# Performance work log

Measured on AMD Instinct MI355X. Metric: run time of the kernel, lower is better.

Reference implementation:

```python
import jax, jax.numpy as jnp
import numpy as np

NUM_EMBED = 1024
NUM_HEADS = 16
NUM_LAYER = 8
BLOCK_SIZE = 1024
VOCAB = 32000
B, T = 4, 1024
HEAD_SIZE = NUM_EMBED // NUM_HEADS


def _ln(x, g, b, eps=1e-5):
    mu = jnp.mean(x, axis=-1, keepdims=True)
    var = jnp.var(x, axis=-1, keepdims=True)
    return (x - mu) * jax.lax.rsqrt(var + eps) * g + b


def setup_inputs() -> dict:
    key = jax.random.key(0)
    ks = jax.random.split(key, 16)
    C, L, V = NUM_EMBED, NUM_LAYER, VOCAB
    std = 0.02
    n = lambda k, shp: jax.random.normal(k, shp, jnp.float32) * std
    return {
        "x": jax.random.randint(ks[0], (B, T), 0, V),
        "tok_emb": n(ks[1], (V, C)),
        "pos_emb": n(ks[2], (BLOCK_SIZE, C)),
        "Wq": n(ks[3], (L, C, C)),
        "Wk": n(ks[4], (L, C, C)),
        "Wv": n(ks[5], (L, C, C)),
        "Wproj": n(ks[6], (L, C, C)),
        "bproj": jnp.zeros((L, C), jnp.float32),
        "ln1_g": jnp.ones((L, C), jnp.float32),
        "ln1_b": jnp.zeros((L, C), jnp.float32),
        "ln2_g": jnp.ones((L, C), jnp.float32),
        "ln2_b": jnp.zeros((L, C), jnp.float32),
        "W1": n(ks[7], (L, C, 4 * C)),
        "b1": jnp.zeros((L, 4 * C), jnp.float32),
        "W2": n(ks[8], (L, 4 * C, C)),
        "b2": jnp.zeros((L, C), jnp.float32),
        "lnf_g": jnp.ones((C,), jnp.float32),
        "lnf_b": jnp.zeros((C,), jnp.float32),
        "Whead": n(ks[9], (C, V)),
    }


def _forward(x, tok_emb, pos_emb, Wq, Wk, Wv, Wproj, bproj,
             ln1_g, ln1_b, ln2_g, ln2_b, W1, b1, W2, b2,
             lnf_g, lnf_b, Whead):
    Bc, Tc = x.shape
    H, hs = NUM_HEADS, HEAD_SIZE
    h = tok_emb[x] + pos_emb[:Tc]  # [B,T,C]
    causal = jnp.tril(jnp.ones((Tc, Tc), bool))
    neg_inf = jnp.finfo(h.dtype).min
    for l in range(NUM_LAYER):
        xn = _ln(h, ln1_g[l], ln1_b[l])
        q = (xn @ Wq[l]).reshape(Bc, Tc, H, hs)
        k = (xn @ Wk[l]).reshape(Bc, Tc, H, hs)
        v = (xn @ Wv[l]).reshape(Bc, Tc, H, hs)
        att = jnp.einsum('bqhd,bkhd->bhqk', q, k) * (hs ** -0.5)
        att = jnp.where(causal, att, neg_inf)
        att = jax.nn.softmax(att, axis=-1)  # dropout p=0 in eval
        o = jnp.einsum('bhqk,bkhd->bqhd', att, v).reshape(Bc, Tc, H * hs)
        h = h + o @ Wproj[l] + bproj[l]
        xn = _ln(h, ln2_g[l], ln2_b[l])
        h = h + jax.nn.relu(xn @ W1[l] + b1[l]) @ W2[l] + b2[l]
    h = _ln(h, lnf_g, lnf_b)
    return h @ Whead  # logits [B,T,V]


def reference(x, tok_emb, pos_emb, Wq, Wk, Wv, Wproj, bproj,
              ln1_g, ln1_b, ln2_g, ln2_b, W1, b1, W2, b2,
              lnf_g, lnf_b, Whead):
    return _forward(x, tok_emb, pos_emb, Wq, Wk, Wv, Wproj, bproj,
                    ln1_g, ln1_b, ln2_g, ln2_b, W1, b1, W2, b2,
                    lnf_g, lnf_b, Whead)
```

## Files before the change

kernel.cpp:

```cpp
#include <hip/hip_runtime.h>
#include <stdint.h>
#include <stddef.h>

#define C_DIM 1024
#define T_DIM 1024
#define B_DIM 4
#define L_DIM 8
#define V_DIM 32000
#define HS 64
#define NHEAD 16
#define NROWS (B_DIM * T_DIM)
#define LDQ   3072

typedef __bf16 bf16_t;
typedef __attribute__((ext_vector_type(8))) __bf16 bf16x8;
typedef __attribute__((ext_vector_type(4))) __bf16 bf16x4;
typedef __attribute__((ext_vector_type(4))) float f32x4;
typedef unsigned int u32;
typedef unsigned short u16;

static __device__ __forceinline__ f32x4 mfma16(bf16x8 a, bf16x8 b, f32x4 c) {
    return __builtin_amdgcn_mfma_f32_16x16x32_bf16(a, b, c, 0, 0, 0);
}

static __device__ __forceinline__ void gl_lds16(const bf16_t* g, bf16_t* l) {
    __builtin_amdgcn_global_load_lds(
        (const __attribute__((address_space(1))) u32*)(const void*)g,
        (__attribute__((address_space(3))) u32*)(void*)l, 16, 0, 0);
}

__global__ __launch_bounds__(256) void embed_kernel(
    const int* __restrict__ x, const float* __restrict__ tok,
    const float* __restrict__ pos, float* __restrict__ h) {
    int idx = blockIdx.x * 256 + threadIdx.x;
    int row = idx >> 8;
    int c4  = (idx & 255) * 4;
    int t   = row & (T_DIM - 1);
    int tk  = x[row];
    float4 a = *(const float4*)(tok + (size_t)tk * C_DIM + c4);
    float4 p = *(const float4*)(pos + (size_t)t * C_DIM + c4);
    float4 r;
    r.x = a.x + p.x; r.y = a.y + p.y; r.z = a.z + p.z; r.w = a.w + p.w;
    *(float4*)(h + (size_t)row * C_DIM + c4) = r;
}

static __device__ __forceinline__ void wtr_tile(
    const float* __restrict__ in, bf16_t* __restrict__ out,
    int K, int N, int n0, int k0, int tid) {
    __shared__ float t[64][65];
    int tx = tid & 63, tw = tid >> 6;
#pragma unroll 4
    for (int i = 0; i < 16; ++i) {
        int k = tw * 16 + i;
        t[k][tx] = in[(size_t)(k0 + k) * N + n0 + tx];
    }
    __syncthreads();
#pragma unroll 4
    for (int i = 0; i < 16; ++i) {
        int n = tw * 16 + i;
        out[(size_t)(n0 + n) * K + k0 + tx] = (bf16_t)t[tx][n];
    }
}

__global__ __launch_bounds__(256) void wtr_kernel(
    const float* __restrict__ in, bf16_t* __restrict__ out, int K, int N) {
    wtr_tile(in, out, K, N, blockIdx.x * 64, blockIdx.y * 64, threadIdx.x);
}

__global__ __launch_bounds__(256) void wtr_layer_kernel(
    const float* __restrict__ Wq, const float* __restrict__ Wk,
    const float* __restrict__ Wv, const float* __restrict__ Wp,
    const float* __restrict__ W1, const float* __restrict__ W2,
    bf16_t* __restrict__ qkvT, bf16_t* __restrict__ projT,
    bf16_t* __restrict__ w1T, bf16_t* __restrict__ w2T) {
    int b = blockIdx.x;
    const float* in; bf16_t* out; int K, N, tn, tk;
    if (b < 1024) {
        int which = b >> 8, t = b & 255;
        in  = which == 0 ? Wq : which == 1 ? Wk : which == 2 ? Wv : Wp;
        out = which < 3 ? qkvT + (size_t)which * C_DIM * C_DIM : projT;
        K = C_DIM; N = C_DIM; tn = t & 15; tk = t >> 4;
    } else if (b < 2048) {
        int t = b - 1024; in = W1; out = w1T;
        K = C_DIM; N = 4 * C_DIM; tn = t & 63; tk = t >> 6;
    } else {
        int t = b - 2048; in = W2; out = w2T;
        K = 4 * C_DIM; N = C_DIM; tn = t & 15; tk = t >> 4;
    }
    wtr_tile(in, out, K, N, tn * 64, tk * 64, threadIdx.x);
}

__global__ __launch_bounds__(256) void ln_kernel(
    const float* __restrict__ x, const float* __restrict__ gam,
    const float* __restrict__ bet, bf16_t* __restrict__ out) {
    int wave = threadIdx.x >> 6, lane = threadIdx.x & 63;
    int row  = blockIdx.x * 4 + wave;
    const float* xr = x + (size_t)row * C_DIM;
    float4 v[4];
    float s = 0.f, sq = 0.f;
#pragma unroll
    for (int i = 0; i < 4; ++i) {
        v[i] = *(const float4*)(xr + i * 256 + lane * 4);
        s  += v[i].x + v[i].y + v[i].z + v[i].w;
        sq += v[i].x * v[i].x + v[i].y * v[i].y + v[i].z * v[i].z + v[i].w * v[i].w;
    }
#pragma unroll
    for (int m = 1; m < 64; m <<= 1) {
        s  += __shfl_xor(s, m);
        sq += __shfl_xor(sq, m);
    }
    float mu  = s * (1.f / 1024.f);
    float var = sq * (1.f / 1024.f) - mu * mu;
    float rs  = rsqrtf(var + 1e-5f);
    bf16_t* orow = out + (size_t)row * C_DIM;
#pragma unroll
    for (int i = 0; i < 4; ++i) {
        int c = i * 256 + lane * 4;
        float4 g4 = *(const float4*)(gam + c);
        float4 b4 = *(const float4*)(bet + c);
        bf16x4 o;
        o[0] = (bf16_t)((v[i].x - mu) * rs * g4.x + b4.x);
        o[1] = (bf16_t)((v[i].y - mu) * rs * g4.y + b4.y);
        o[2] = (bf16_t)((v[i].z - mu) * rs * g4.z + b4.z);
        o[3] = (bf16_t)((v[i].w - mu) * rs * g4.w + b4.w);
        *(bf16x4*)(orow + c) = o;
    }
}

template <int MODE>
__global__ __launch_bounds__(256) void gemm_kernel(
    const bf16_t* __restrict__ A, const bf16_t* __restrict__ Bt,
    const float* __restrict__ bias, void* __restrict__ Cout,
    int M, int N, int K) {
    __shared__ bf16_t Asm[2][128 * 32];
    __shared__ bf16_t Bsm[2][128 * 32];

    const int tid  = threadIdx.x;
    const int nwg  = gridDim.x;
    int bid = blockIdx.x;
    if ((nwg & 7) == 0) {
        int cpx = nwg >> 3;
        bid = (bid & 7) * cpx + (bid >> 3);
    }
    const int MT = M >> 7;
    const int mt = bid % MT, nt = bid / MT;
    const int mbase = mt << 7, nbase = nt << 7;
    const int wave = tid >> 6, lane = tid & 63;
    const int lr = lane & 15, lg = lane >> 4;
    const int wm = wave >> 1, wn = wave & 1;
    const int NK = K >> 5;

    const int srow = lane >> 2;
    const int ssw  = (((lane & 3) ^ ((lane >> 3) & 3)) << 3);
    const bf16_t* aRow = A  + (size_t)(mbase + wave * 32 + srow) * K + ssw;
    const bf16_t* bRow = Bt + (size_t)(nbase + wave * 32 + srow) * K + ssw;
    const int ldsW = wave * 1024;

#define STAGE(buf, kt)                                                        \
    do {                                                                      \
        const bf16_t* ag = aRow + (size_t)(kt) * 32;                          \
        const bf16_t* bg = bRow + (size_t)(kt) * 32;                          \
        gl_lds16(ag,            &Asm[buf][ldsW]);                             \
        gl_lds16(ag + 16 * K,   &Asm[buf][ldsW + 512]);                       \
        gl_lds16(bg,            &Bsm[buf][ldsW]);                             \
        gl_lds16(bg + 16 * K,   &Bsm[buf][ldsW + 512]);                       \
    } while (0)

    STAGE(0, 0);
    __syncthreads();

    f32x4 acc[4][4] = {};
    const int rsw = ((lg ^ ((lr >> 1) & 3)) << 3);
    int buf = 0;
    for (int kt = 0; kt < NK; ++kt) {
        if (kt + 1 < NK) STAGE(buf ^ 1, kt + 1);
        bf16x8 af[4], bfr[4];
#pragma unroll
        for (int i = 0; i < 4; ++i)
            af[i] = *(const bf16x8*)&Asm[buf][(wm * 64 + i * 16 + lr) * 32 + rsw];
#pragma unroll
        for (int j = 0; j < 4; ++j)
            bfr[j] = *(const bf16x8*)&Bsm[buf][(wn * 64 + j * 16 + lr) * 32 + rsw];
#pragma unroll
        for (int i = 0; i < 4; ++i)
#pragma unroll
            for (int j = 0; j < 4; ++j)
                acc[i][j] = mfma16(af[i], bfr[j], acc[i][j]);
        __syncthreads();
        buf ^= 1;
    }
#undef STAGE

    float bj[4];
#pragma unroll
    for (int j = 0; j < 4; ++j)
        bj[j] = bias ? bias[nbase + wn * 64 + j * 16 + lr] : 0.0f;
#pragma unroll
    for (int i = 0; i < 4; ++i) {
#pragma unroll
        for (int j = 0; j < 4; ++j) {
            int col = nbase + wn * 64 + j * 16 + lr;
#pragma unroll
            for (int e = 0; e < 4; ++e) {
                int row = mbase + wm * 64 + i * 16 + lg * 4 + e;
                float val = acc[i][j][e] + bj[j];
                size_t off = (size_t)row * N + col;
                if (MODE == 0) {
                    ((bf16_t*)Cout)[off] = (bf16_t)val;
                } else if (MODE == 1) {
                    ((bf16_t*)Cout)[off] = (bf16_t)fmaxf(val, 0.0f);
                } else if (MODE == 2) {
                    ((float*)Cout)[off] += val;
                } else {
                    __builtin_nontemporal_store(val, &((float*)Cout)[off]);
                }
            }
        }
    }
}

template <int MODE>
__global__ __launch_bounds__(512, 2) void gemm256_kernel(
    const bf16_t* __restrict__ A, const bf16_t* __restrict__ Bt,
    const float* __restrict__ bias, void* __restrict__ Cout,
    int M, int N, int K) {
    __shared__ bf16_t As[2][256 * 64];
    __shared__ bf16_t Bs[2][256 * 64];

    const int tid  = threadIdx.x;
    const int nwg  = gridDim.x;
    int bid = blockIdx.x;
    if ((nwg & 7) == 0) {
        int cpx = nwg >> 3;
        bid = (bid & 7) * cpx + (bid >> 3);
    }
    const int MT = M >> 8;
    const int mt = bid % MT, nt = bid / MT;
    const int mbase = mt << 8, nbase = nt << 8;
    const int wave = tid >> 6, lane = tid & 63;
    const int lr = lane & 15, lg = lane >> 4;
    const int wm128 = (wave >> 2) * 128;
    const int wn64  = (wave & 3) * 64;
    const int NT = K >> 6;

    const int ssw = (((tid & 7) ^ ((tid >> 3) & 7)) << 3);
    const bf16_t* aRow = A  + (size_t)(mbase + (tid >> 3)) * K + ssw;
    const bf16_t* bRow = Bt + (size_t)(nbase + (tid >> 3)) * K + ssw;
    const int ldsW = wave * 8 * 64;

#pragma unroll
    for (int i = 0; i < 4; ++i) {
        gl_lds16(aRow + (size_t)i * 64 * K, &As[0][i * 64 * 64 + ldsW]);
        gl_lds16(bRow + (size_t)i * 64 * K, &Bs[0][i * 64 * 64 + ldsW]);
    }
    asm volatile("s_waitcnt vmcnt(0)" ::: "memory");
    __builtin_amdgcn_s_barrier();
    asm volatile("" ::: "memory");

    f32x4 acc[8][4] = {};

    for (int t = 0; t < NT; ++t) {
        const int cur = t & 1, nxt = cur ^ 1;
        const bool pf = (t + 1 < NT);
#pragma unroll
        for (int q = 0; q < 4; ++q) {
            bf16x8 af[2][2], bfr[2][4];
#pragma unroll
            for (int h = 0; h < 2; ++h) {
                const int c = h * 4 + lg;
#pragma unroll
                for (int dm = 0; dm < 2; ++dm) {
                    int row = wm128 + (2 * q + dm) * 16 + lr;
                    af[h][dm] = *(const bf16x8*)
                        &As[cur][row * 64 + ((c ^ (row & 7)) << 3)];
                }
#pragma unroll
                for (int nf = 0; nf < 4; ++nf) {
                    int row = wn64 + nf * 16 + lr;
                    bfr[h][nf] = *(const bf16x8*)
                        &Bs[cur][row * 64 + ((c ^ (row & 7)) << 3)];
                }
            }
            if (q < 2 && pf) {
#pragma unroll
                for (int i = 2 * q; i < 2 * q + 2; ++i) {
                    gl_lds16(aRow + (size_t)(t + 1) * 64 + (size_t)i * 64 * K,
                             &As[nxt][i * 64 * 64 + ldsW]);
                    gl_lds16(bRow + (size_t)(t + 1) * 64 + (size_t)i * 64 * K,
                             &Bs[nxt][i * 64 * 64 + ldsW]);
                }
            }
            __builtin_amdgcn_s_barrier();
            asm volatile("" ::: "memory");
            __builtin_amdgcn_s_setprio(1);
#pragma unroll
            for (int h = 0; h < 2; ++h)
#pragma unroll
                for (int dm = 0; dm < 2; ++dm)
#pragma unroll
                    for (int nf = 0; nf < 4; ++nf)
                        acc[2 * q + dm][nf] =
                            mfma16(af[h][dm], bfr[h][nf], acc[2 * q + dm][nf]);
            __builtin_amdgcn_s_setprio(0);
            __builtin_amdgcn_s_barrier();
            asm volatile("" ::: "memory");
        }
        if (pf) asm volatile("s_waitcnt vmcnt(0)" ::: "memory");
        __builtin_amdgcn_s_barrier();
        asm volatile("" ::: "memory");
    }

    float bj[4];
#pragma unroll
    for (int nf = 0; nf < 4; ++nf)
        bj[nf] = bias ? bias[nbase + wn64 + nf * 16 + lr] : 0.0f;
#pragma unroll
    for (int mf = 0; mf < 8; ++mf) {
#pragma unroll
        for (int nf = 0; nf < 4; ++nf) {
            int col = nbase + wn64 + nf * 16 + lr;
#pragma unroll
            for (int e = 0; e < 4; ++e) {
                int row = mbase + wm128 + mf * 16 + lg * 4 + e;
                float val = acc[mf][nf][e] + bj[nf];
                size_t off = (size_t)row * N + col;
                if (MODE == 1) {
                    ((bf16_t*)Cout)[off] = (bf16_t)fmaxf(val, 0.0f);
                } else {
                    __builtin_nontemporal_store(val, &((float*)Cout)[off]);
                }
            }
        }
    }
}

__global__ __launch_bounds__(256) void attn_kernel(
    const bf16_t* __restrict__ Qb, const bf16_t* __restrict__ Kb,
    const bf16_t* __restrict__ Vb, bf16_t* __restrict__ Ob) {
    __shared__ bf16_t Ksm[2][64][72];
    __shared__ bf16_t Vsm[2][64][72];
    __shared__ bf16_t Psm[4][32][72];

    const int tid  = threadIdx.x;
    const int bid  = blockIdx.x;
    const int qt   = 7 - (bid >> 6);
    const int bh   = bid & 63;
    const int hh   = bh & 15;
    const int bb   = bh >> 4;
    const int wave = tid >> 6, lane = tid & 63;
    const int lr = lane & 15, lg = lane >> 4;
    const int qbase = qt * 128 + wave * 32;
    const size_t basei = ((size_t)bb * T_DIM) * LDQ + hh * HS;
    const size_t baseo = ((size_t)bb * T_DIM) * C_DIM + hh * HS;

    bf16x8 qf[2][2];
#pragma unroll
    for (int rb = 0; rb < 2; ++rb) {
        const bf16_t* qrow = Qb + basei + (size_t)(qbase + rb * 16 + lr) * LDQ;
        qf[rb][0] = *(const bf16x8*)(qrow + lg * 8);
        qf[rb][1] = *(const bf16x8*)(qrow + 32 + lg * 8);
    }

    f32x4 o[2][4] = {};
    float m_run[2][4], psum[2][4];
#pragma unroll
    for (int rb = 0; rb < 2; ++rb)
#pragma unroll
        for (int e = 0; e < 4; ++e) { m_run[rb][e] = -1e30f; psum[rb][e] = 0.f; }

    const int krow = tid >> 2, kc = (tid & 3) * 8;
    const bf16_t* kgp = Kb + basei + (size_t)krow * LDQ + kc;
    const int vds = (tid & 7) * 8, vkg = (tid >> 3) * 2;
    const bf16_t* vgp0 = Vb + basei + (size_t)vkg * LDQ + vds;
    const bf16_t* vgp1 = vgp0 + LDQ;

    const int nkt = 2 * qt + 2;

    uint4 k0r, k1r, v0r, v1r;
    k0r = *(const uint4*)(kgp);
    k1r = *(const uint4*)(kgp + 32);
    v0r = *(const uint4*)(vgp0);
    v1r = *(const uint4*)(vgp1);
    *(uint4*)&Ksm[0][krow][kc]      = k0r;
    *(uint4*)&Ksm[0][krow][kc + 32] = k1r;
    {
        const u16* e0 = (const u16*)&v0r;
        const u16* e1 = (const u16*)&v1r;
#pragma unroll
        for (int j = 0; j < 8; ++j)
            *(u32*)&Vsm[0][vds + j][vkg] = (u32)e0[j] | ((u32)e1[j] << 16);
    }
    __syncthreads();

    const float SCL = 0.18033688011112042f;
    for (int kt = 0; kt < nkt; ++kt) {
        const int c = kt & 1;
        if (kt + 1 < nkt) {
            const size_t go = (size_t)(kt + 1) * 64 * LDQ;
            k0r = *(const uint4*)(kgp + go);
            k1r = *(const uint4*)(kgp + go + 32);
            v0r = *(const uint4*)(vgp0 + go);
            v1r = *(const uint4*)(vgp1 + go);
        }

        f32x4 s[2][4];
        __builtin_amdgcn_s_setprio(1);
#pragma unroll
        for (int kk = 0; kk < 4; ++kk) {
            bf16x8 kf0 = *(const bf16x8*)&Ksm[c][kk * 16 + lr][lg * 8];
            bf16x8 kf1 = *(const bf16x8*)&Ksm[c][kk * 16 + lr][32 + lg * 8];
#pragma unroll
            for (int rb = 0; rb < 2; ++rb) {
                f32x4 z = {};
                z = mfma16(qf[rb][0], kf0, z);
                z = mfma16(qf[rb][1], kf1, z);
                s[rb][kk] = z;
            }
        }
        __builtin_amdgcn_s_setprio(0);
        if (kt * 64 + 63 > qbase) {
#pragma unroll
            for (int rb = 0; rb < 2; ++rb)
#pragma unroll
                for (int kk = 0; kk < 4; ++kk)
#pragma unroll
                    for (int e = 0; e < 4; ++e) {
                        int key = kt * 64 + kk * 16 + lr;
                        int qi  = qbase + rb * 16 + lg * 4 + e;
                        float v = s[rb][kk][e] * SCL;
                        s[rb][kk][e] = (key <= qi) ? v : -1e30f;
                    }
        } else {
#pragma unroll
            for (int rb = 0; rb < 2; ++rb)
#pragma unroll
                for (int kk = 0; kk < 4; ++kk)
#pragma unroll
                    for (int e = 0; e < 4; ++e)
                        s[rb][kk][e] *= SCL;
        }

#pragma unroll
        for (int rb = 0; rb < 2; ++rb) {
#pragma unroll
            for (int e = 0; e < 4; ++e) {
                float v = fmaxf(fmaxf(s[rb][0][e], s[rb][1][e]),
                                fmaxf(s[rb][2][e], s[rb][3][e]));
                v = fmaxf(v, __shfl_xor(v, 1));
                v = fmaxf(v, __shfl_xor(v, 2));
                v = fmaxf(v, __shfl_xor(v, 4));
                v = fmaxf(v, __shfl_xor(v, 8));
                float mo = m_run[rb][e];
                if (v > mo + 8.f) {
                    float alpha = exp2f(mo - v);
                    m_run[rb][e] = v;
                    psum[rb][e] *= alpha;
#pragma unroll
                    for (int db = 0; db < 4; ++db)
                        o[rb][db][e] *= alpha;
                }
                float mn = m_run[rb][e];
                float p0 = exp2f(s[rb][0][e] - mn);
                float p1 = exp2f(s[rb][1][e] - mn);
                float p2 = exp2f(s[rb][2][e] - mn);
                float p3 = exp2f(s[rb][3][e] - mn);
                int qrow = rb * 16 + lg * 4 + e;
                Psm[wave][qrow][lr]      = (bf16_t)p0;
                Psm[wave][qrow][16 + lr] = (bf16_t)p1;
                Psm[wave][qrow][32 + lr] = (bf16_t)p2;
                Psm[wave][qrow][48 + lr] = (bf16_t)p3;
                psum[rb][e] += (p0 + p1) + (p2 + p3);
            }
        }

        asm volatile("s_waitcnt lgkmcnt(0)" ::: "memory");
        bf16x8 pf[2][2];
#pragma unroll
        for (int rb = 0; rb < 2; ++rb)
#pragma unroll
            for (int h2 = 0; h2 < 2; ++h2)
                pf[rb][h2] = *(const bf16x8*)&Psm[wave][rb * 16 + lr][h2 * 32 + lg * 8];
        __builtin_amdgcn_s_setprio(1);
#pragma unroll
        for (int h2 = 0; h2 < 2; ++h2)
#pragma unroll
            for (int db = 0; db < 4; ++db) {
                bf16x8 vf = *(const bf16x8*)&Vsm[c][db * 16 + lr][h2 * 32 + lg * 8];
#pragma unroll
                for (int rb = 0; rb < 2; ++rb)
                    o[rb][db] = mfma16(pf[rb][h2], vf, o[rb][db]);
            }
        __builtin_amdgcn_s_setprio(0);

        if (kt + 1 < nkt) {
            const int w = c ^ 1;
            *(uint4*)&Ksm[w][krow][kc]      = k0r;
            *(uint4*)&Ksm[w][krow][kc + 32] = k1r;
            const u16* e0 = (const u16*)&v0r;
            const u16* e1 = (const u16*)&v1r;
#pragma unroll
            for (int j = 0; j < 8; ++j)
                *(u32*)&Vsm[w][vds + j][vkg] = (u32)e0[j] | ((u32)e1[j] << 16);
        }
        __syncthreads();
    }

#pragma unroll
    for (int rb = 0; rb < 2; ++rb)
#pragma unroll
        for (int e = 0; e < 4; ++e) {
            float l = psum[rb][e];
            l += __shfl_xor(l, 1);
            l += __shfl_xor(l, 2);
            l += __shfl_xor(l, 4);
            l += __shfl_xor(l, 8);
            float inv = 1.0f / l;
            bf16_t* orow = Ob + baseo + (size_t)(qbase + rb * 16 + lg * 4 + e) * C_DIM;
#pragma unroll
            for (int db = 0; db < 4; ++db)
                orow[db * 16 + lr] = (bf16_t)(o[rb][db][e] * inv);
        }
}

extern "C" void kernel_launch(void* const* d_in, const int* in_sizes, int n_in,
                              void* d_out, int out_size, void* d_ws, size_t ws_size,
                              hipStream_t stream) {
    const int*   x      = (const int*)d_in[0];
    const float* tok    = (const float*)d_in[1];
    const float* pos    = (const float*)d_in[2];
    const float* Wq     = (const float*)d_in[3];
    const float* Wk     = (const float*)d_in[4];
    const float* Wv     = (const float*)d_in[5];
    const float* Wproj  = (const float*)d_in[6];
    const float* bproj  = (const float*)d_in[7];
    const float* ln1_g  = (const float*)d_in[8];
    const float* ln1_b  = (const float*)d_in[9];
    const float* ln2_g  = (const float*)d_in[10];
    const float* ln2_b  = (const float*)d_in[11];
    const float* W1     = (const float*)d_in[12];
    const float* b1     = (const float*)d_in[13];
    const float* W2     = (const float*)d_in[14];
    const float* b2     = (const float*)d_in[15];
    const float* lnf_g  = (const float*)d_in[16];
    const float* lnf_b  = (const float*)d_in[17];
    const float* Whead  = (const float*)d_in[18];
    float* out = (float*)d_out;

    char* ws = (char*)d_ws;
    float*  h    = (float*)ws;   ws += (size_t)NROWS * C_DIM * 4;
    bf16_t* xn   = (bf16_t*)ws;  ws += (size_t)NROWS * C_DIM * 2;
    bf16_t* qkvb = (bf16_t*)ws;  ws += (size_t)NROWS * LDQ * 2;
    bf16_t* ob   = (bf16_t*)ws;  ws += (size_t)NROWS * C_DIM * 2;
    bf16_t* mid  = (bf16_t*)ws;  ws += (size_t)NROWS * 4 * C_DIM * 2;
    bf16_t* wT   = (bf16_t*)ws;  ws += (size_t)V_DIM * C_DIM * 2;

    const size_t M1 = (size_t)C_DIM * C_DIM;
    bf16_t* qkvT  = wT;
    bf16_t* projT = wT + 3 * M1;
    bf16_t* w1T   = wT + 4 * M1;
    bf16_t* w2T   = wT + 8 * M1;

    dim3 blk(256);
    dim3 blk512(512);

    embed_kernel<<<dim3(NROWS * C_DIM / 1024), blk, 0, stream>>>(x, tok, pos, h);

    for (int l = 0; l < L_DIM; ++l) {
        const size_t wo  = (size_t)l * M1;
        const size_t wo1 = (size_t)l * 4 * M1;

        wtr_layer_kernel<<<dim3(3072), blk, 0, stream>>>(
            Wq + wo, Wk + wo, Wv + wo, Wproj + wo, W1 + wo1, W2 + wo1,
            qkvT, projT, w1T, w2T);

        ln_kernel<<<dim3(NROWS / 4), blk, 0, stream>>>(h, ln1_g + l * C_DIM, ln1_b + l * C_DIM, xn);

        gemm_kernel<0><<<dim3(32 * 24), blk, 0, stream>>>(xn, qkvT, nullptr, qkvb, NROWS, LDQ, C_DIM);

        attn_kernel<<<dim3(B_DIM * NHEAD * (T_DIM / 128)), blk, 0, stream>>>(
            qkvb, qkvb + C_DIM, qkvb + 2 * C_DIM, ob);

        gemm_kernel<2><<<dim3(32 * 8), blk, 0, stream>>>(ob, projT, bproj + l * C_DIM, h, NROWS, C_DIM, C_DIM);

        ln_kernel<<<dim3(NROWS / 4), blk, 0, stream>>>(h, ln2_g + l * C_DIM, ln2_b + l * C_DIM, xn);

        gemm256_kernel<1><<<dim3(16 * 16), blk512, 0, stream>>>(
            xn, w1T, b1 + (size_t)l * 4 * C_DIM, mid, NROWS, 4 * C_DIM, C_DIM);
        gemm_kernel<2><<<dim3(32 * 8), blk, 0, stream>>>(mid, w2T, b2 + l * C_DIM, h, NROWS, C_DIM, 4 * C_DIM);
    }

    ln_kernel<<<dim3(NROWS / 4), blk, 0, stream>>>(h, lnf_g, lnf_b, xn);
    wtr_kernel<<<dim3(500, 16), blk, 0, stream>>>(Whead, wT, C_DIM, V_DIM);
    gemm256_kernel<3><<<dim3(16 * 125), blk512, 0, stream>>>(
        xn, wT, nullptr, out, NROWS, V_DIM, C_DIM);
}
```

Measured before the change: 2.677 ms.

## Batch all weight transposes into one launch, swizzle attention LDS, trim GEMM barrier

All per-layer weight transposes and the LM-head transpose now run in a single up-front kernel whenever the workspace is large enough, replacing nine separate launches and the serialization between them. The attention kernel's V and P shared-memory tiles get rotated/XOR-style column swizzles to reduce LDS bank conflicts on the MFMA operand reads. The GEMM inner loop also drops the trailing barrier after the last sub-step, since a barrier follows anyway. The up-front transpose path needs much more workspace and falls back to the old path when that is not available.

```diff
diff --git a/kernel.cpp b/kernel.cpp
--- a/kernel.cpp
+++ b/kernel.cpp
@@ -90,6 +90,41 @@
     wtr_tile(in, out, K, N, tn * 64, tk * 64, threadIdx.x);
 }
 
+__global__ __launch_bounds__(256) void wtr_all_kernel(
+    const float* __restrict__ Wq, const float* __restrict__ Wk,
+    const float* __restrict__ Wv, const float* __restrict__ Wp,
+    const float* __restrict__ W1, const float* __restrict__ W2,
+    const float* __restrict__ Wh,
+    bf16_t* __restrict__ wAll, bf16_t* __restrict__ headT) {
+    const size_t M1 = (size_t)C_DIM * C_DIM;
+    int b = blockIdx.x;
+    if (b < 24576) {
+        int l = b / 3072, r = b % 3072;
+        const size_t wo  = (size_t)l * M1;
+        const size_t wo1 = (size_t)l * 4 * M1;
+        bf16_t* lw = wAll + (size_t)l * 12 * M1;
+        const float* in; bf16_t* out; int K, N, tn, tk;
+        if (r < 1024) {
+            int which = r >> 8, t = r & 255;
+            in  = (which == 0 ? Wq + wo : which == 1 ? Wk + wo :
+                   which == 2 ? Wv + wo : Wp + wo);
+            out = which < 3 ? lw + (size_t)which * M1 : lw + 3 * M1;
+            K = C_DIM; N = C_DIM; tn = t & 15; tk = t >> 4;
+        } else if (r < 2048) {
+            int t = r - 1024; in = W1 + wo1; out = lw + 4 * M1;
+            K = C_DIM; N = 4 * C_DIM; tn = t & 63; tk = t >> 6;
+        } else {
+            int t = r - 2048; in = W2 + wo1; out = lw + 8 * M1;
+            K = 4 * C_DIM; N = C_DIM; tn = t & 15; tk = t >> 4;
+        }
+        wtr_tile(in, out, K, N, tn * 64, tk * 64, threadIdx.x);
+    } else {
+        int b2 = b - 24576;
+        int tn = b2 % 500, tk = b2 / 500;
+        wtr_tile(Wh, headT, C_DIM, V_DIM, tn * 64, tk * 64, threadIdx.x);
+    }
+}
+
 __global__ __launch_bounds__(256) void ln_kernel(
     const float* __restrict__ x, const float* __restrict__ gam,
     const float* __restrict__ bet, bf16_t* __restrict__ out) {
@@ -302,8 +337,10 @@
                         acc[2 * q + dm][nf] =
                             mfma16(af[h][dm], bfr[h][nf], acc[2 * q + dm][nf]);
             __builtin_amdgcn_s_setprio(0);
-            __builtin_amdgcn_s_barrier();
-            asm volatile("" ::: "memory");
+            if (q < 3) {
+                __builtin_amdgcn_s_barrier();
+                asm volatile("" ::: "memory");
+            }
         }
         if (pf) asm volatile("s_waitcnt vmcnt(0)" ::: "memory");
         __builtin_amdgcn_s_barrier();
@@ -371,6 +408,7 @@
     const int krow = tid >> 2, kc = (tid & 3) * 8;
     const bf16_t* kgp = Kb + basei + (size_t)krow * LDQ + kc;
     const int vds = (tid & 7) * 8, vkg = (tid >> 3) * 2;
+    const int vcol = ((((vkg >> 3) + (tid & 7)) & 7) << 3) + (vkg & 7);
     const bf16_t* vgp0 = Vb + basei + (size_t)vkg * LDQ + vds;
     const bf16_t* vgp1 = vgp0 + LDQ;
 
@@ -388,7 +426,7 @@
         const u16* e1 = (const u16*)&v1r;
 #pragma unroll
         for (int j = 0; j < 8; ++j)
-            *(u32*)&Vsm[0][vds + j][vkg] = (u32)e0[j] | ((u32)e1[j] << 16);
+            *(u32*)&Vsm[0][vds + j][vcol] = (u32)e0[j] | ((u32)e1[j] << 16);
     }
     __syncthreads();
 
@@ -465,10 +503,11 @@
                 float p2 = exp2f(s[rb][2][e] - mn);
                 float p3 = exp2f(s[rb][3][e] - mn);
                 int qrow = rb * 16 + lg * 4 + e;
-                Psm[wave][qrow][lr]      = (bf16_t)p0;
-                Psm[wave][qrow][16 + lr] = (bf16_t)p1;
-                Psm[wave][qrow][32 + lr] = (bf16_t)p2;
-                Psm[wave][qrow][48 + lr] = (bf16_t)p3;
+                int rot  = qrow >> 2;
+                Psm[wave][qrow][((0 + rot) & 3) * 16 + lr] = (bf16_t)p0;
+                Psm[wave][qrow][((1 + rot) & 3) * 16 + lr] = (bf16_t)p1;
+                Psm[wave][qrow][((2 + rot) & 3) * 16 + lr] = (bf16_t)p2;
+                Psm[wave][qrow][((3 + rot) & 3) * 16 + lr] = (bf16_t)p3;
                 psum[rb][e] += (p0 + p1) + (p2 + p3);
             }
         }
@@ -476,16 +515,24 @@
         asm volatile("s_waitcnt lgkmcnt(0)" ::: "memory");
         bf16x8 pf[2][2];
 #pragma unroll
-        for (int rb = 0; rb < 2; ++rb)
-#pragma unroll
-            for (int h2 = 0; h2 < 2; ++h2)
-                pf[rb][h2] = *(const bf16x8*)&Psm[wave][rb * 16 + lr][h2 * 32 + lg * 8];
+        for (int rb = 0; rb < 2; ++rb) {
+            int prow = rb * 16 + lr;
+            int prot = prow >> 2;
+#pragma unroll
+            for (int h2 = 0; h2 < 2; ++h2) {
+                int pg = ((2 * h2 + (lg >> 1)) + prot) & 3;
+                pf[rb][h2] = *(const bf16x8*)
+                    &Psm[wave][prow][pg * 16 + (lg & 1) * 8];
+            }
+        }
         __builtin_amdgcn_s_setprio(1);
 #pragma unroll
         for (int h2 = 0; h2 < 2; ++h2)
 #pragma unroll
             for (int db = 0; db < 4; ++db) {
-                bf16x8 vf = *(const bf16x8*)&Vsm[c][db * 16 + lr][h2 * 32 + lg * 8];
+                int vr  = db * 16 + lr;
+                int vpc = ((h2 * 4 + lg) + (vr >> 3)) & 7;
+                bf16x8 vf = *(const bf16x8*)&Vsm[c][vr][vpc << 3];
 #pragma unroll
                 for (int rb = 0; rb < 2; ++rb)
                     o[rb][db] = mfma16(pf[rb][h2], vf, o[rb][db]);
@@ -500,7 +547,7 @@
             const u16* e1 = (const u16*)&v1r;
 #pragma unroll
             for (int j = 0; j < 8; ++j)
-                *(u32*)&Vsm[w][vds + j][vkg] = (u32)e0[j] | ((u32)e1[j] << 16);
+                *(u32*)&Vsm[w][vds + j][vcol] = (u32)e0[j] | ((u32)e1[j] << 16);
         }
         __syncthreads();
     }
@@ -546,32 +593,48 @@
     const float* Whead  = (const float*)d_in[18];
     float* out = (float*)d_out;
 
+    const size_t M1 = (size_t)C_DIM * C_DIM;
     char* ws = (char*)d_ws;
     float*  h    = (float*)ws;   ws += (size_t)NROWS * C_DIM * 4;
     bf16_t* xn   = (bf16_t*)ws;  ws += (size_t)NROWS * C_DIM * 2;
     bf16_t* qkvb = (bf16_t*)ws;  ws += (size_t)NROWS * LDQ * 2;
     bf16_t* ob   = (bf16_t*)ws;  ws += (size_t)NROWS * C_DIM * 2;
     bf16_t* mid  = (bf16_t*)ws;  ws += (size_t)NROWS * 4 * C_DIM * 2;
-    bf16_t* wT   = (bf16_t*)ws;  ws += (size_t)V_DIM * C_DIM * 2;
-
-    const size_t M1 = (size_t)C_DIM * C_DIM;
-    bf16_t* qkvT  = wT;
-    bf16_t* projT = wT + 3 * M1;
-    bf16_t* w1T   = wT + 4 * M1;
-    bf16_t* w2T   = wT + 8 * M1;
+
+    const size_t used_act = (size_t)(ws - (char*)d_ws);
+    const size_t need_big = used_act + (8 * 12 * M1 + (size_t)V_DIM * C_DIM) * 2;
+    const bool big = ws_size >= need_big;
+
+    bf16_t* wAll = nullptr; bf16_t* headT = nullptr; bf16_t* wT = nullptr;
+    if (big) {
+        wAll  = (bf16_t*)ws;  ws += 8 * 12 * M1 * 2;
+        headT = (bf16_t*)ws;  ws += (size_t)V_DIM * C_DIM * 2;
+    } else {
+        wT    = (bf16_t*)ws;  ws += (size_t)V_DIM * C_DIM * 2;
+    }
 
     dim3 blk(256);
     dim3 blk512(512);
 
     embed_kernel<<<dim3(NROWS * C_DIM / 1024), blk, 0, stream>>>(x, tok, pos, h);
+    if (big)
+        wtr_all_kernel<<<dim3(24576 + 8000), blk, 0, stream>>>(
+            Wq, Wk, Wv, Wproj, W1, W2, Whead, wAll, headT);
 
     for (int l = 0; l < L_DIM; ++l) {
         const size_t wo  = (size_t)l * M1;
         const size_t wo1 = (size_t)l * 4 * M1;
 
-        wtr_layer_kernel<<<dim3(3072), blk, 0, stream>>>(
-            Wq + wo, Wk + wo, Wv + wo, Wproj + wo, W1 + wo1, W2 + wo1,
-            qkvT, projT, w1T, w2T);
+        bf16_t *qkvT, *projT, *w1T, *w2T;
+        if (big) {
+            bf16_t* lw = wAll + (size_t)l * 12 * M1;
+            qkvT = lw; projT = lw + 3 * M1; w1T = lw + 4 * M1; w2T = lw + 8 * M1;
+        } else {
+            qkvT = wT; projT = wT + 3 * M1; w1T = wT + 4 * M1; w2T = wT + 8 * M1;
+            wtr_layer_kernel<<<dim3(3072), blk, 0, stream>>>(
+                Wq + wo, Wk + wo, Wv + wo, Wproj + wo, W1 + wo1, W2 + wo1,
+                qkvT, projT, w1T, w2T);
+        }
 
         ln_kernel<<<dim3(NROWS / 4), blk, 0, stream>>>(h, ln1_g + l * C_DIM, ln1_b + l * C_DIM, xn);
 
@@ -590,7 +653,10 @@
     }
 
     ln_kernel<<<dim3(NROWS / 4), blk, 0, stream>>>(h, lnf_g, lnf_b, xn);
-    wtr_kernel<<<dim3(500, 16), blk, 0, stream>>>(Whead, wT, C_DIM, V_DIM);
+    if (!big) {
+        wtr_kernel<<<dim3(500, 16), blk, 0, stream>>>(Whead, wT, C_DIM, V_DIM);
+        headT = wT;
+    }
     gemm256_kernel<3><<<dim3(16 * 125), blk512, 0, stream>>>(
-        xn, wT, nullptr, out, NROWS, V_DIM, C_DIM);
-}
+        xn, headT, nullptr, out, NROWS, V_DIM, C_DIM);
+}
```

Measured after the change: 3.172 ms. 18.5% more time.
